# Optimization experiments

Measured on AMD Instinct MI355X. Metric: run time of the kernel, lower is better.

Reference implementation:

```python
import jax, jax.numpy as jnp
import numpy as np

N = 100000      # nodes
E = 1600000     # edges
IN_DIM = 500
HID = 64
OUT = 40
BN_EPS = 1e-5


def setup_inputs() -> dict:
    key = jax.random.key(0)
    ks = jax.random.split(key, 20)
    x = jax.random.normal(ks[0], (N, IN_DIM), dtype=jnp.float32)
    edge_index = jax.random.randint(ks[1], (2, E), 0, N, dtype=jnp.int64)

    def lin(k, fin, fout):
        return jax.random.normal(k, (fin, fout), dtype=jnp.float32) / np.sqrt(fin).astype(np.float32)

    inp = {
        "x": x,
        "edge_index": edge_index,
        "W1": lin(ks[2], IN_DIM, HID),
        "b1": jnp.zeros((HID,), jnp.float32),
        "g1": jnp.ones((HID,), jnp.float32),
        "be1": jnp.zeros((HID,), jnp.float32),
        "m1": 0.1 * jax.random.normal(ks[3], (HID,), jnp.float32),
        "v1": jax.random.uniform(ks[4], (HID,), jnp.float32, 0.5, 1.5),
        "W2": lin(ks[5], HID, HID),
        "b2": jnp.zeros((HID,), jnp.float32),
        "g2": jnp.ones((HID,), jnp.float32),
        "be2": jnp.zeros((HID,), jnp.float32),
        "m2": 0.1 * jax.random.normal(ks[6], (HID,), jnp.float32),
        "v2": jax.random.uniform(ks[7], (HID,), jnp.float32, 0.5, 1.5),
        "W3": lin(ks[8], HID, OUT),
        "b3": jnp.zeros((OUT,), jnp.float32),
    }
    return inp


def _gcn_conv(h, src, dst, deg_inv_sqrt, W, b):
    # PyG GCNConv (add_self_loops=True, normalize=True, eval math):
    # out = D^-1/2 (A + I) D^-1/2 (h @ W) + b
    h = h @ W                                    # [N, F]
    norm = deg_inv_sqrt[src] * deg_inv_sqrt[dst]  # [E]
    msg = h[src] * norm[:, None]                  # [E, F] gather
    agg = jax.ops.segment_sum(msg, dst, num_segments=N)  # scatter-add
    agg = agg + h * (deg_inv_sqrt * deg_inv_sqrt)[:, None]  # self-loop term
    return agg + b


def reference(x, edge_index, W1, b1, g1, be1, m1, v1,
              W2, b2, g2, be2, m2, v2, W3, b3):
    src, dst = edge_index[0], edge_index[1]
    # degree including self-loop
    deg = jax.ops.segment_sum(jnp.ones((E,), x.dtype), dst, num_segments=N) + 1.0
    deg_inv_sqrt = jax.lax.rsqrt(deg)

    def bn(h, g, be, m, v):
        return (h - m) * jax.lax.rsqrt(v + BN_EPS) * g + be

    h = _gcn_conv(x, src, dst, deg_inv_sqrt, W1, b1)
    h = jax.nn.relu(bn(h, g1, be1, m1, v1))
    # dropout: identity in eval mode
    h = _gcn_conv(h, src, dst, deg_inv_sqrt, W2, b2)
    h = jax.nn.relu(bn(h, g2, be2, m2, v2))
    out = _gcn_conv(h, src, dst, deg_inv_sqrt, W3, b3)
    return jax.nn.log_softmax(out, axis=1)
```

## Files before the change

kernel.cpp:

```cpp
#include <hip/hip_runtime.h>
#include <math.h>

#define N_NODES 100000
#define N_EDGES 1600000
#define IN_DIM  500
#define HID     64
#define OUT_DIM 40
#define BN_EPS  1e-5f
#define SCAN_NB 98
#define NTILE   6250

typedef _Float16 f16;
typedef __attribute__((ext_vector_type(2))) _Float16 f16x2;
typedef __attribute__((ext_vector_type(8))) _Float16 f16x8;
typedef __attribute__((ext_vector_type(4))) float f32x4;

static inline int cdiv(long a, int b) { return (int)((a + b - 1) / b); }

__device__ inline unsigned short f2h_bits(float f) {
    f16 h = (f16)f;
    return __builtin_bit_cast(unsigned short, h);
}
__device__ inline f16x2 bits2h2(unsigned int u) {
    return __builtin_bit_cast(f16x2, u);
}

__global__ void k_count_deg(const int* __restrict__ ei, int* degi) {
    int e = blockIdx.x * 256 + threadIdx.x;
    if (e < N_EDGES) atomicAdd(&degi[ei[N_EDGES + e]], 1);
}

__global__ void k_scan1(const int* __restrict__ degi, int* __restrict__ rowptr,
                        int* __restrict__ blocksum, float* __restrict__ dis) {
    __shared__ int sd[256];
    int tid = threadIdx.x;
    int base = blockIdx.x * 1024 + tid * 4;
    int v0 = (base + 0 < N_NODES) ? degi[base + 0] : -1;
    int v1 = (base + 1 < N_NODES) ? degi[base + 1] : -1;
    int v2 = (base + 2 < N_NODES) ? degi[base + 2] : -1;
    int v3 = (base + 3 < N_NODES) ? degi[base + 3] : -1;
    if (base + 0 < N_NODES) dis[base + 0] = rsqrtf((float)v0 + 1.0f);
    if (base + 1 < N_NODES) dis[base + 1] = rsqrtf((float)v1 + 1.0f);
    if (base + 2 < N_NODES) dis[base + 2] = rsqrtf((float)v2 + 1.0f);
    if (base + 3 < N_NODES) dis[base + 3] = rsqrtf((float)v3 + 1.0f);
    int w0 = v0 + 1, w1 = v1 + 1, w2 = v2 + 1, w3 = v3 + 1;
    int s = w0 + w1 + w2 + w3;
    sd[tid] = s;
    __syncthreads();
    for (int off = 1; off < 256; off <<= 1) {
        int t = (tid >= off) ? sd[tid - off] : 0;
        __syncthreads();
        sd[tid] += t;
        __syncthreads();
    }
    int excl = sd[tid] - s;
    if (base + 0 < N_NODES) rowptr[base + 0] = excl;
    if (base + 1 < N_NODES) rowptr[base + 1] = excl + w0;
    if (base + 2 < N_NODES) rowptr[base + 2] = excl + w0 + w1;
    if (base + 3 < N_NODES) rowptr[base + 3] = excl + w0 + w1 + w2;
    if (tid == 255) blocksum[blockIdx.x] = sd[255];
}

__global__ void k_scan2(int* __restrict__ blocksum, int* __restrict__ blockbase) {
    __shared__ int sd[128];
    int tid = threadIdx.x;
    int v = (tid < SCAN_NB) ? blocksum[tid] : 0;
    sd[tid] = v;
    __syncthreads();
    for (int off = 1; off < 128; off <<= 1) {
        int t = (tid >= off) ? sd[tid - off] : 0;
        __syncthreads();
        sd[tid] += t;
        __syncthreads();
    }
    if (tid < SCAN_NB) blockbase[tid] = sd[tid] - v;
}

__global__ void k_scan3(int* __restrict__ rowptr, const int* __restrict__ blockbase,
                        const int* __restrict__ degi, int* __restrict__ cursor,
                        uint2* __restrict__ epack) {
    int add = blockbase[blockIdx.x];
    int base = blockIdx.x * 1024 + threadIdx.x * 4;
#pragma unroll
    for (int i = 0; i < 4; ++i) {
        int node = base + i;
        if (node < N_NODES) {
            int rp = rowptr[node] + add;
            rowptr[node] = rp;
            float d2 = 1.0f / (float)(degi[node] + 1);
            unsigned int hb = f2h_bits(d2);
            epack[rp] = make_uint2((unsigned int)(node * 128), (hb << 16) | hb);
            cursor[node] = 1;
        }
    }
    if (blockIdx.x == 0 && threadIdx.x == 0)
        rowptr[N_NODES] = N_EDGES + N_NODES;
}

__global__ void k_permute(const int* __restrict__ ei, const int* __restrict__ rowptr,
                          int* __restrict__ cursor, const float* __restrict__ dis,
                          uint2* __restrict__ epack) {
    int e = blockIdx.x * 256 + threadIdx.x;
    if (e >= N_EDGES) return;
    int s = ei[e];
    int d = ei[N_EDGES + e];
    int pos = rowptr[d] + atomicAdd(&cursor[d], 1);
    unsigned int hb = f2h_bits(dis[s] * dis[d]);
    epack[pos] = make_uint2((unsigned int)(s * 128), (hb << 16) | hb);
}

__device__ inline void convW_one(const float* W, unsigned short* wb,
                                 int idx, int K, int F) {
    int j    = idx & 7;
    int lane = (idx >> 3) & 63;
    int q    = idx >> 9;
    int t    = q >> 2, nt = q & 3;
    int n = nt * 16 + (lane & 15);
    int k = t * 32 + ((lane >> 4) << 3) + j;
    float v = (k < K && n < F) ? W[(long)k * F + n] : 0.f;
    wb[idx] = f2h_bits(v);
}

__global__ void k_convall(const float* __restrict__ W1, const float* __restrict__ W2,
                          const float* __restrict__ W3,
                          unsigned short* __restrict__ wb1,
                          unsigned short* __restrict__ wb2,
                          unsigned short* __restrict__ wb3) {
    int idx = blockIdx.x * 256 + threadIdx.x;
    if (idx < 32768) {
        convW_one(W1, wb1, idx, IN_DIM, HID);
    } else if (idx < 36864) {
        convW_one(W2, wb2, idx - 32768, HID, HID);
    } else {
        convW_one(W3, wb3, idx - 36864, HID, OUT_DIM);
    }
}

__global__ void k_bnfold(const float* __restrict__ b1, const float* __restrict__ g1,
                         const float* __restrict__ be1, const float* __restrict__ m1,
                         const float* __restrict__ v1,
                         const float* __restrict__ b2, const float* __restrict__ g2,
                         const float* __restrict__ be2, const float* __restrict__ m2,
                         const float* __restrict__ v2,
                         unsigned short* __restrict__ sc1,
                         unsigned short* __restrict__ sc2) {
    int t = threadIdx.x;
    int c = t & 63;
    const float *b, *g, *be, *m, *v;
    unsigned short* sc;
    if (t < 64) { b = b1; g = g1; be = be1; m = m1; v = v1; sc = sc1; }
    else        { b = b2; g = g2; be = be2; m = m2; v = v2; sc = sc2; }
    float S = g[c] * rsqrtf(v[c] + BN_EPS);
    float C = (b[c] - m[c]) * S + be[c];
    sc[c]      = f2h_bits(S);
    sc[64 + c] = f2h_bits(C);
}

__global__ __launch_bounds__(256) void k_l1fused(
        const float* __restrict__ x,
        const unsigned short* __restrict__ wb,
        unsigned short* __restrict__ h) {
    __shared__ unsigned short l[16 * 520];
    const int rt = blockIdx.x;
    const int tid = threadIdx.x;

#pragma unroll
    for (int it = 0; it < 8; ++it) {
        int slot = it * 256 + tid;
        int row = slot >> 7, kq = slot & 127;
        float4 v = make_float4(0.f, 0.f, 0.f, 0.f);
        if (kq < 125)
            v = *reinterpret_cast<const float4*>(x + ((long)rt * 16 + row) * IN_DIM + kq * 4);
        unsigned int u0 = (unsigned int)f2h_bits(v.x) | ((unsigned int)f2h_bits(v.y) << 16);
        unsigned int u1 = (unsigned int)f2h_bits(v.z) | ((unsigned int)f2h_bits(v.w) << 16);
        *reinterpret_cast<uint2*>(&l[row * 520 + kq * 4]) = make_uint2(u0, u1);
    }
    __syncthreads();

    const int wid  = tid >> 6;
    const int lane = tid & 63;
    const int l15  = lane & 15;
    const int lhi  = lane >> 4;

    const f16x8* bp = reinterpret_cast<const f16x8*>(wb) + wid * 64 + lane;
    const unsigned short* arow = &l[l15 * 520 + lhi * 8];

    f32x4 acc = (f32x4){0.f, 0.f, 0.f, 0.f};
    f16x8 ca = *reinterpret_cast<const f16x8*>(arow);
    f16x8 cb = bp[0];

#pragma unroll
    for (int t = 0; t < 16; ++t) {
        f16x8 na, nb;
        if (t < 15) {
            na = *reinterpret_cast<const f16x8*>(arow + (t + 1) * 32);
            nb = bp[(t + 1) * 256];
        }
        acc = __builtin_amdgcn_mfma_f32_16x16x32_f16(ca, cb, acc, 0, 0, 0);
        if (t < 15) { ca = na; cb = nb; }
    }

#pragma unroll
    for (int rr = 0; rr < 4; ++rr) {
        long grow = (long)rt * 16 + lhi * 4 + rr;
        h[grow * 64 + wid * 16 + l15] = f2h_bits(acc[rr]);
    }
}

__global__ __launch_bounds__(256) void k_agg_gemm(
        const unsigned short* __restrict__ h_in, const int* __restrict__ rowptr,
        const uint2* __restrict__ epack, const unsigned short* __restrict__ sc,
        const unsigned short* __restrict__ wb, unsigned short* __restrict__ h_out) {
    __shared__ unsigned short st[16 * 80];
    const int base = blockIdx.x * 16;
    const int tid  = threadIdx.x;
    const int wid  = tid >> 6;
    const int lane = tid & 63;
    const int e8 = lane >> 3, c8 = lane & 7;
    const int node0 = base + wid * 4;

    int start[4], cnt[4];
    {
        int r0 = rowptr[node0 + 0], r1 = rowptr[node0 + 1], r2 = rowptr[node0 + 2];
        int r3 = rowptr[node0 + 3], r4 = rowptr[node0 + 4];
        start[0] = r0; cnt[0] = r1 - r0;
        start[1] = r1; cnt[1] = r2 - r1;
        start[2] = r2; cnt[2] = r3 - r2;
        start[3] = r3; cnt[3] = r4 - r3;
    }
    const char* hb = (const char*)h_in + c8 * 16;

    f16x2 a[4][4];
#pragma unroll
    for (int s = 0; s < 4; ++s)
#pragma unroll
        for (int i = 0; i < 4; ++i) a[s][i] = (f16x2)0;

    int maxc = max(max(cnt[0], cnt[1]), max(cnt[2], cnt[3]));

    for (int j = 0; j < maxc; j += 8) {
        int jj = j + e8;
#pragma unroll
        for (int s = 0; s < 4; ++s) {
            bool valid = jj < cnt[s];
            uint2 mv = epack[start[s] + (valid ? jj : 0)];
            f16x2 w2 = bits2h2(valid ? mv.y : 0u);
            uint4 hv = *(const uint4*)(hb + mv.x);
            a[s][0] += bits2h2(hv.x) * w2;
            a[s][1] += bits2h2(hv.y) * w2;
            a[s][2] += bits2h2(hv.z) * w2;
            a[s][3] += bits2h2(hv.w) * w2;
        }
    }

#pragma unroll
    for (int off = 8; off < 64; off <<= 1) {
#pragma unroll
        for (int s = 0; s < 4; ++s)
#pragma unroll
            for (int i = 0; i < 4; ++i) {
                unsigned int u = __builtin_bit_cast(unsigned int, a[s][i]);
                a[s][i] += bits2h2((unsigned int)__shfl_xor((int)u, off));
            }
    }

    if (e8 == 0) {
        uint4 Su = *(const uint4*)(sc + c8 * 8);
        uint4 Cu = *(const uint4*)(sc + 64 + c8 * 8);
        unsigned int sw[4] = {Su.x, Su.y, Su.z, Su.w};
        unsigned int cw[4] = {Cu.x, Cu.y, Cu.z, Cu.w};
#pragma unroll
        for (int s = 0; s < 4; ++s) {
            unsigned int u[4];
#pragma unroll
            for (int p = 0; p < 4; ++p) {
                f16x2 r = a[s][p] * bits2h2(sw[p]) + bits2h2(cw[p]);
                r[0] = r[0] > (f16)0 ? r[0] : (f16)0;
                r[1] = r[1] > (f16)0 ? r[1] : (f16)0;
                u[p] = __builtin_bit_cast(unsigned int, r);
            }
            int row = wid * 4 + s;
            *reinterpret_cast<uint4*>(&st[row * 80 + c8 * 8]) =
                make_uint4(u[0], u[1], u[2], u[3]);
        }
    }
    __syncthreads();

    const int l15 = lane & 15, lhi = lane >> 4;
    const unsigned short* arow = &st[l15 * 80 + lhi * 8];
    const f16x8* bp = reinterpret_cast<const f16x8*>(wb) + wid * 64 + lane;

    f32x4 acc = (f32x4){0.f, 0.f, 0.f, 0.f};
    f16x8 a0 = *reinterpret_cast<const f16x8*>(arow);
    f16x8 a1 = *reinterpret_cast<const f16x8*>(arow + 32);
    f16x8 b0 = bp[0];
    f16x8 b1 = bp[256];
    acc = __builtin_amdgcn_mfma_f32_16x16x32_f16(a0, b0, acc, 0, 0, 0);
    acc = __builtin_amdgcn_mfma_f32_16x16x32_f16(a1, b1, acc, 0, 0, 0);

#pragma unroll
    for (int rr = 0; rr < 4; ++rr) {
        long grow = (long)base + lhi * 4 + rr;
        h_out[grow * 64 + wid * 16 + l15] = f2h_bits(acc[rr]);
    }
}

__global__ __launch_bounds__(256) void k_agg_lsm(
        const unsigned short* __restrict__ h, const int* __restrict__ rowptr,
        const uint2* __restrict__ epack,
        const float* __restrict__ bias, float* __restrict__ out) {
    int node = blockIdx.x * 4 + (threadIdx.x >> 6);
    if (node >= N_NODES) return;
    const int lane = threadIdx.x & 63;
    const int e8 = lane >> 3, c8 = lane & 7;
    const bool okc = c8 < 5;

    const int start = rowptr[node];
    const int cnt   = rowptr[node + 1] - start;
    const uint2* ep = epack + start;
    const char*  hb = (const char*)h + c8 * 16;

    f16x2 a[4] = {(f16x2)0, (f16x2)0, (f16x2)0, (f16x2)0};

    auto batch = [&](int j) {
        int jj = j + e8;
        bool valid = jj < cnt;
        uint2 mv = ep[valid ? jj : 0];
        f16x2 w2 = bits2h2((valid && okc) ? mv.y : 0u);
        uint4 hv = *(const uint4*)(hb + (okc ? mv.x : 0u));
        a[0] += bits2h2(hv.x) * w2;
        a[1] += bits2h2(hv.y) * w2;
        a[2] += bits2h2(hv.z) * w2;
        a[3] += bits2h2(hv.w) * w2;
    };

    batch(0);
    if (cnt > 8)  batch(8);
    if (cnt > 16) batch(16);
    if (cnt > 24) batch(24);
    for (int j = 32; j < cnt; j += 8) batch(j);

#pragma unroll
    for (int off = 8; off < 64; off <<= 1) {
#pragma unroll
        for (int i = 0; i < 4; ++i) {
            unsigned int u = __builtin_bit_cast(unsigned int, a[i]);
            a[i] += bits2h2((unsigned int)__shfl_xor((int)u, off));
        }
    }

    float av[8] = {(float)a[0][0], (float)a[0][1], (float)a[1][0], (float)a[1][1],
                   (float)a[2][0], (float)a[2][1], (float)a[3][0], (float)a[3][1]};
    float vals[8];
    float mx = -INFINITY;
    if (okc) {
        float4 bb0 = *(const float4*)(bias + c8 * 8), bb1 = *(const float4*)(bias + c8 * 8 + 4);
        float bbv[8] = {bb0.x, bb0.y, bb0.z, bb0.w, bb1.x, bb1.y, bb1.z, bb1.w};
#pragma unroll
        for (int i = 0; i < 8; ++i) {
            vals[i] = av[i] + bbv[i];
            mx = fmaxf(mx, vals[i]);
        }
    }
#pragma unroll
    for (int o = 1; o < 8; o <<= 1) mx = fmaxf(mx, __shfl_xor(mx, o));
    float es = 0.f;
    if (okc) {
#pragma unroll
        for (int i = 0; i < 8; ++i) es += expf(vals[i] - mx);
    }
#pragma unroll
    for (int o = 1; o < 8; o <<= 1) es += __shfl_xor(es, o);
    float ls = logf(es);

    if (e8 == 0 && okc) {
        float* op = out + (long)node * 40 + c8 * 8;
        *(float4*)op = make_float4(vals[0] - mx - ls, vals[1] - mx - ls,
                                   vals[2] - mx - ls, vals[3] - mx - ls);
        *(float4*)(op + 4) = make_float4(vals[4] - mx - ls, vals[5] - mx - ls,
                                         vals[6] - mx - ls, vals[7] - mx - ls);
    }
}

extern "C" void kernel_launch(void* const* d_in, const int* in_sizes, int n_in,
                              void* d_out, int out_size, void* d_ws, size_t ws_size,
                              hipStream_t stream) {
    const float* x   = (const float*)d_in[0];
    const int*   ei  = (const int*)d_in[1];
    const float* W1  = (const float*)d_in[2];
    const float* b1  = (const float*)d_in[3];
    const float* g1  = (const float*)d_in[4];
    const float* be1 = (const float*)d_in[5];
    const float* m1  = (const float*)d_in[6];
    const float* v1  = (const float*)d_in[7];
    const float* W2  = (const float*)d_in[8];
    const float* b2  = (const float*)d_in[9];
    const float* g2  = (const float*)d_in[10];
    const float* be2 = (const float*)d_in[11];
    const float* m2  = (const float*)d_in[12];
    const float* v2  = (const float*)d_in[13];
    const float* W3  = (const float*)d_in[14];
    const float* b3  = (const float*)d_in[15];
    float* out = (float*)d_out;

    float* ws        = (float*)d_ws;
    float* dis       = ws;
    int*   degi      = (int*)(ws + 100096);
    int*   cursor    = (int*)(ws + 200192);
    int*   rowptr    = (int*)(ws + 300288);
    int*   blocksum  = (int*)(ws + 400384);
    int*   blockbase = (int*)(ws + 400512);
    uint2* epack     = (uint2*)(ws + 400640);
    unsigned short* h1 = (unsigned short*)(ws + 3800640);
    unsigned short* h2 = (unsigned short*)(ws + 7000640);
    unsigned short* h3 = (unsigned short*)(ws + 10200640);
    unsigned short* wb1 = (unsigned short*)(ws + 13400640);
    unsigned short* wb2 = (unsigned short*)(ws + 13417024);
    unsigned short* wb3 = (unsigned short*)(ws + 13419072);
    unsigned short* sc1 = (unsigned short*)(ws + 13421120);
    unsigned short* sc2 = sc1 + 128;

    hipMemsetAsync(degi, 0, 100096 * sizeof(int), stream);
    k_count_deg<<<cdiv(N_EDGES, 256), 256, 0, stream>>>(ei, degi);
    k_scan1<<<SCAN_NB, 256, 0, stream>>>(degi, rowptr, blocksum, dis);
    k_scan2<<<1, 128, 0, stream>>>(blocksum, blockbase);
    k_scan3<<<SCAN_NB, 256, 0, stream>>>(rowptr, blockbase, degi, cursor, epack);
    k_permute<<<cdiv(N_EDGES, 256), 256, 0, stream>>>(ei, rowptr, cursor, dis, epack);

    k_convall<<<160, 256, 0, stream>>>(W1, W2, W3, wb1, wb2, wb3);
    k_bnfold<<<1, 128, 0, stream>>>(b1, g1, be1, m1, v1, b2, g2, be2, m2, v2, sc1, sc2);

    const int agg_grid = cdiv(N_NODES, 4);

    k_l1fused<<<NTILE, 256, 0, stream>>>(x, wb1, h1);

    k_agg_gemm<<<NTILE, 256, 0, stream>>>(h1, rowptr, epack, sc1, wb2, h2);

    k_agg_gemm<<<NTILE, 256, 0, stream>>>(h2, rowptr, epack, sc2, wb3, h3);

    k_agg_lsm<<<agg_grid, 256, 0, stream>>>(h3, rowptr, epack, b3, out);
}
```

Before: 335.4 us.

## Overlap layer-1 GEMM with CSR build phases and restructure aggregation loop

Splits the layer-1 dense projection into three chunks and co-schedules each chunk in the same launch as a graph preprocessing phase: degree counting, the scan finalize, and the edge permutation. The latency-bound atomic phases can then overlap with the bandwidth-heavy x read. Weight conversion and BN folding are merged into one launch, cutting launch count. The aggregation loop now walks each node's edges separately instead of iterating all four nodes up to the max degree, which avoids padded gathers but loses interleaved memory-level parallelism across nodes.

```diff
diff --git a/kernel.cpp b/kernel.cpp
--- a/kernel.cpp
+++ b/kernel.cpp
@@ -9,6 +9,10 @@
 #define BN_EPS  1e-5f
 #define SCAN_NB 98
 #define NTILE   6250
+#define EBLK    6250
+#define L1A     2500
+#define L1B     1250
+#define L1C     2500
 
 typedef _Float16 f16;
 typedef __attribute__((ext_vector_type(2))) _Float16 f16x2;
@@ -23,11 +27,6 @@
 }
 __device__ inline f16x2 bits2h2(unsigned int u) {
     return __builtin_bit_cast(f16x2, u);
-}
-
-__global__ void k_count_deg(const int* __restrict__ ei, int* degi) {
-    int e = blockIdx.x * 256 + threadIdx.x;
-    if (e < N_EDGES) atomicAdd(&degi[ei[N_EDGES + e]], 1);
 }
 
 __global__ void k_scan1(const int* __restrict__ degi, int* __restrict__ rowptr,
@@ -76,11 +75,12 @@
     if (tid < SCAN_NB) blockbase[tid] = sd[tid] - v;
 }
 
-__global__ void k_scan3(int* __restrict__ rowptr, const int* __restrict__ blockbase,
-                        const int* __restrict__ degi, int* __restrict__ cursor,
-                        uint2* __restrict__ epack) {
-    int add = blockbase[blockIdx.x];
-    int base = blockIdx.x * 1024 + threadIdx.x * 4;
+__device__ inline void dev_scan3(int bid, int tid, int* __restrict__ rowptr,
+                                 const int* __restrict__ blockbase,
+                                 const int* __restrict__ degi, int* __restrict__ cursor,
+                                 uint2* __restrict__ epack) {
+    int add = blockbase[bid];
+    int base = bid * 1024 + tid * 4;
 #pragma unroll
     for (int i = 0; i < 4; ++i) {
         int node = base + i;
@@ -93,20 +93,107 @@
             cursor[node] = 1;
         }
     }
-    if (blockIdx.x == 0 && threadIdx.x == 0)
+    if (bid == 0 && tid == 0)
         rowptr[N_NODES] = N_EDGES + N_NODES;
 }
 
-__global__ void k_permute(const int* __restrict__ ei, const int* __restrict__ rowptr,
-                          int* __restrict__ cursor, const float* __restrict__ dis,
-                          uint2* __restrict__ epack) {
-    int e = blockIdx.x * 256 + threadIdx.x;
-    if (e >= N_EDGES) return;
-    int s = ei[e];
-    int d = ei[N_EDGES + e];
-    int pos = rowptr[d] + atomicAdd(&cursor[d], 1);
-    unsigned int hb = f2h_bits(dis[s] * dis[d]);
-    epack[pos] = make_uint2((unsigned int)(s * 128), (hb << 16) | hb);
+__device__ inline void dev_l1fused(int rt, int tid,
+                                   const float* __restrict__ x,
+                                   const unsigned short* __restrict__ wb,
+                                   unsigned short* __restrict__ h,
+                                   unsigned short* l ) {
+#pragma unroll
+    for (int it = 0; it < 8; ++it) {
+        int slot = it * 256 + tid;
+        int row = slot >> 7, kq = slot & 127;
+        float4 v = make_float4(0.f, 0.f, 0.f, 0.f);
+        if (kq < 125)
+            v = *reinterpret_cast<const float4*>(x + ((long)rt * 16 + row) * IN_DIM + kq * 4);
+        unsigned int u0 = (unsigned int)f2h_bits(v.x) | ((unsigned int)f2h_bits(v.y) << 16);
+        unsigned int u1 = (unsigned int)f2h_bits(v.z) | ((unsigned int)f2h_bits(v.w) << 16);
+        *reinterpret_cast<uint2*>(&l[row * 520 + kq * 4]) = make_uint2(u0, u1);
+    }
+    __syncthreads();
+
+    const int wid  = tid >> 6;
+    const int lane = tid & 63;
+    const int l15  = lane & 15;
+    const int lhi  = lane >> 4;
+
+    const f16x8* bp = reinterpret_cast<const f16x8*>(wb) + wid * 64 + lane;
+    const unsigned short* arow = &l[l15 * 520 + lhi * 8];
+
+    f32x4 acc = (f32x4){0.f, 0.f, 0.f, 0.f};
+    f16x8 ca = *reinterpret_cast<const f16x8*>(arow);
+    f16x8 cb = bp[0];
+
+#pragma unroll
+    for (int t = 0; t < 16; ++t) {
+        f16x8 na, nb;
+        if (t < 15) {
+            na = *reinterpret_cast<const f16x8*>(arow + (t + 1) * 32);
+            nb = bp[(t + 1) * 256];
+        }
+        acc = __builtin_amdgcn_mfma_f32_16x16x32_f16(ca, cb, acc, 0, 0, 0);
+        if (t < 15) { ca = na; cb = nb; }
+    }
+
+#pragma unroll
+    for (int rr = 0; rr < 4; ++rr) {
+        long grow = (long)rt * 16 + lhi * 4 + rr;
+        h[grow * 64 + wid * 16 + l15] = f2h_bits(acc[rr]);
+    }
+}
+
+__global__ __launch_bounds__(256) void k_front1(
+        const float* __restrict__ x, const unsigned short* __restrict__ wb1,
+        unsigned short* __restrict__ h1,
+        const int* __restrict__ ei, int* __restrict__ degi) {
+    __shared__ unsigned short l[16 * 520];
+    int b = blockIdx.x;
+    if (b < L1A) {
+        dev_l1fused(b, threadIdx.x, x, wb1, h1, l);
+    } else {
+        int e = (b - L1A) * 256 + threadIdx.x;
+        if (e < N_EDGES) atomicAdd(&degi[ei[N_EDGES + e]], 1);
+    }
+}
+
+__global__ __launch_bounds__(256) void k_front2(
+        const float* __restrict__ x, const unsigned short* __restrict__ wb1,
+        unsigned short* __restrict__ h1,
+        int* __restrict__ rowptr, const int* __restrict__ blockbase,
+        const int* __restrict__ degi, int* __restrict__ cursor,
+        uint2* __restrict__ epack) {
+    __shared__ unsigned short l[16 * 520];
+    int b = blockIdx.x;
+    if (b < L1B) {
+        dev_l1fused(L1A + b, threadIdx.x, x, wb1, h1, l);
+    } else {
+        dev_scan3(b - L1B, threadIdx.x, rowptr, blockbase, degi, cursor, epack);
+    }
+}
+
+__global__ __launch_bounds__(256) void k_front3(
+        const float* __restrict__ x, const unsigned short* __restrict__ wb1,
+        unsigned short* __restrict__ h1,
+        const int* __restrict__ ei, const int* __restrict__ rowptr,
+        int* __restrict__ cursor, const float* __restrict__ dis,
+        uint2* __restrict__ epack) {
+    __shared__ unsigned short l[16 * 520];
+    int b = blockIdx.x;
+    if (b < L1C) {
+        dev_l1fused(L1A + L1B + b, threadIdx.x, x, wb1, h1, l);
+    } else {
+        int e = (b - L1C) * 256 + threadIdx.x;
+        if (e < N_EDGES) {
+            int s = ei[e];
+            int d = ei[N_EDGES + e];
+            int pos = rowptr[d] + atomicAdd(&cursor[d], 1);
+            unsigned int hb = f2h_bits(dis[s] * dis[d]);
+            epack[pos] = make_uint2((unsigned int)(s * 128), (hb << 16) | hb);
+        }
+    }
 }
 
 __device__ inline void convW_one(const float* W, unsigned short* wb,
@@ -121,11 +208,34 @@
     wb[idx] = f2h_bits(v);
 }
 
-__global__ void k_convall(const float* __restrict__ W1, const float* __restrict__ W2,
-                          const float* __restrict__ W3,
-                          unsigned short* __restrict__ wb1,
-                          unsigned short* __restrict__ wb2,
-                          unsigned short* __restrict__ wb3) {
+__global__ void k_conv(const float* __restrict__ W1, const float* __restrict__ W2,
+                       const float* __restrict__ W3,
+                       unsigned short* __restrict__ wb1,
+                       unsigned short* __restrict__ wb2,
+                       unsigned short* __restrict__ wb3,
+                       const float* __restrict__ b1, const float* __restrict__ g1,
+                       const float* __restrict__ be1, const float* __restrict__ m1,
+                       const float* __restrict__ v1,
+                       const float* __restrict__ b2, const float* __restrict__ g2,
+                       const float* __restrict__ be2, const float* __restrict__ m2,
+                       const float* __restrict__ v2,
+                       unsigned short* __restrict__ sc1,
+                       unsigned short* __restrict__ sc2) {
+    if (blockIdx.x == 160) {
+        int t = threadIdx.x;
+        if (t < 128) {
+            int c = t & 63;
+            const float *b, *g, *be, *m, *v;
+            unsigned short* sc;
+            if (t < 64) { b = b1; g = g1; be = be1; m = m1; v = v1; sc = sc1; }
+            else        { b = b2; g = g2; be = be2; m = m2; v = v2; sc = sc2; }
+            float S = g[c] * rsqrtf(v[c] + BN_EPS);
+            float C = (b[c] - m[c]) * S + be[c];
+            sc[c]      = f2h_bits(S);
+            sc[64 + c] = f2h_bits(C);
+        }
+        return;
+    }
     int idx = blockIdx.x * 256 + threadIdx.x;
     if (idx < 32768) {
         convW_one(W1, wb1, idx, IN_DIM, HID);
@@ -133,77 +243,6 @@
         convW_one(W2, wb2, idx - 32768, HID, HID);
     } else {
         convW_one(W3, wb3, idx - 36864, HID, OUT_DIM);
-    }
-}
-
-__global__ void k_bnfold(const float* __restrict__ b1, const float* __restrict__ g1,
-                         const float* __restrict__ be1, const float* __restrict__ m1,
-                         const float* __restrict__ v1,
-                         const float* __restrict__ b2, const float* __restrict__ g2,
-                         const float* __restrict__ be2, const float* __restrict__ m2,
-                         const float* __restrict__ v2,
-                         unsigned short* __restrict__ sc1,
-                         unsigned short* __restrict__ sc2) {
-    int t = threadIdx.x;
-    int c = t & 63;
-    const float *b, *g, *be, *m, *v;
-    unsigned short* sc;
-    if (t < 64) { b = b1; g = g1; be = be1; m = m1; v = v1; sc = sc1; }
-    else        { b = b2; g = g2; be = be2; m = m2; v = v2; sc = sc2; }
-    float S = g[c] * rsqrtf(v[c] + BN_EPS);
-    float C = (b[c] - m[c]) * S + be[c];
-    sc[c]      = f2h_bits(S);
-    sc[64 + c] = f2h_bits(C);
-}
-
-__global__ __launch_bounds__(256) void k_l1fused(
-        const float* __restrict__ x,
-        const unsigned short* __restrict__ wb,
-        unsigned short* __restrict__ h) {
-    __shared__ unsigned short l[16 * 520];
-    const int rt = blockIdx.x;
-    const int tid = threadIdx.x;
-
-#pragma unroll
-    for (int it = 0; it < 8; ++it) {
-        int slot = it * 256 + tid;
-        int row = slot >> 7, kq = slot & 127;
-        float4 v = make_float4(0.f, 0.f, 0.f, 0.f);
-        if (kq < 125)
-            v = *reinterpret_cast<const float4*>(x + ((long)rt * 16 + row) * IN_DIM + kq * 4);
-        unsigned int u0 = (unsigned int)f2h_bits(v.x) | ((unsigned int)f2h_bits(v.y) << 16);
-        unsigned int u1 = (unsigned int)f2h_bits(v.z) | ((unsigned int)f2h_bits(v.w) << 16);
-        *reinterpret_cast<uint2*>(&l[row * 520 + kq * 4]) = make_uint2(u0, u1);
-    }
-    __syncthreads();
-
-    const int wid  = tid >> 6;
-    const int lane = tid & 63;
-    const int l15  = lane & 15;
-    const int lhi  = lane >> 4;
-
-    const f16x8* bp = reinterpret_cast<const f16x8*>(wb) + wid * 64 + lane;
-    const unsigned short* arow = &l[l15 * 520 + lhi * 8];
-
-    f32x4 acc = (f32x4){0.f, 0.f, 0.f, 0.f};
-    f16x8 ca = *reinterpret_cast<const f16x8*>(arow);
-    f16x8 cb = bp[0];
-
-#pragma unroll
-    for (int t = 0; t < 16; ++t) {
-        f16x8 na, nb;
-        if (t < 15) {
-            na = *reinterpret_cast<const f16x8*>(arow + (t + 1) * 32);
-            nb = bp[(t + 1) * 256];
-        }
-        acc = __builtin_amdgcn_mfma_f32_16x16x32_f16(ca, cb, acc, 0, 0, 0);
-        if (t < 15) { ca = na; cb = nb; }
-    }
-
-#pragma unroll
-    for (int rr = 0; rr < 4; ++rr) {
-        long grow = (long)rt * 16 + lhi * 4 + rr;
-        h[grow * 64 + wid * 16 + l15] = f2h_bits(acc[rr]);
     }
 }
 
@@ -236,21 +275,25 @@
 #pragma unroll
         for (int i = 0; i < 4; ++i) a[s][i] = (f16x2)0;
 
-    int maxc = max(max(cnt[0], cnt[1]), max(cnt[2], cnt[3]));
-
-    for (int j = 0; j < maxc; j += 8) {
+    auto gath = [&](int s, int j) {
         int jj = j + e8;
-#pragma unroll
-        for (int s = 0; s < 4; ++s) {
-            bool valid = jj < cnt[s];
-            uint2 mv = epack[start[s] + (valid ? jj : 0)];
-            f16x2 w2 = bits2h2(valid ? mv.y : 0u);
-            uint4 hv = *(const uint4*)(hb + mv.x);
-            a[s][0] += bits2h2(hv.x) * w2;
-            a[s][1] += bits2h2(hv.y) * w2;
-            a[s][2] += bits2h2(hv.z) * w2;
-            a[s][3] += bits2h2(hv.w) * w2;
-        }
+        bool valid = jj < cnt[s];
+        uint2 mv = epack[start[s] + (valid ? jj : 0)];
+        f16x2 w2 = bits2h2(valid ? mv.y : 0u);
+        uint4 hv = *(const uint4*)(hb + mv.x);
+        a[s][0] += bits2h2(hv.x) * w2;
+        a[s][1] += bits2h2(hv.y) * w2;
+        a[s][2] += bits2h2(hv.z) * w2;
+        a[s][3] += bits2h2(hv.w) * w2;
+    };
+
+#pragma unroll
+    for (int s = 0; s < 4; ++s) {
+        gath(s, 0);
+        if (cnt[s] > 8)  gath(s, 8);
+        if (cnt[s] > 16) gath(s, 16);
+        if (cnt[s] > 24) gath(s, 24);
+        for (int j = 32; j < cnt[s]; j += 8) gath(s, j);
     }
 
 #pragma unroll
@@ -421,22 +464,24 @@
     unsigned short* sc2 = sc1 + 128;
 
     hipMemsetAsync(degi, 0, 100096 * sizeof(int), stream);
-    k_count_deg<<<cdiv(N_EDGES, 256), 256, 0, stream>>>(ei, degi);
+
+    k_conv<<<161, 256, 0, stream>>>(W1, W2, W3, wb1, wb2, wb3,
+                                    b1, g1, be1, m1, v1, b2, g2, be2, m2, v2,
+                                    sc1, sc2);
+
+    k_front1<<<L1A + EBLK, 256, 0, stream>>>(x, wb1, h1, ei, degi);
+
     k_scan1<<<SCAN_NB, 256, 0, stream>>>(degi, rowptr, blocksum, dis);
     k_scan2<<<1, 128, 0, stream>>>(blocksum, blockbase);
-    k_scan3<<<SCAN_NB, 256, 0, stream>>>(rowptr, blockbase, degi, cursor, epack);
-    k_permute<<<cdiv(N_EDGES, 256), 256, 0, stream>>>(ei, rowptr, cursor, dis, epack);
-
-    k_convall<<<160, 256, 0, stream>>>(W1, W2, W3, wb1, wb2, wb3);
-    k_bnfold<<<1, 128, 0, stream>>>(b1, g1, be1, m1, v1, b2, g2, be2, m2, v2, sc1, sc2);
-
-    const int agg_grid = cdiv(N_NODES, 4);
-
-    k_l1fused<<<NTILE, 256, 0, stream>>>(x, wb1, h1);
+
+    k_front2<<<L1B + SCAN_NB, 256, 0, stream>>>(x, wb1, h1, rowptr, blockbase,
+                                                degi, cursor, epack);
+
+    k_front3<<<L1C + EBLK, 256, 0, stream>>>(x, wb1, h1, ei, rowptr, cursor,
+                                             dis, epack);
 
     k_agg_gemm<<<NTILE, 256, 0, stream>>>(h1, rowptr, epack, sc1, wb2, h2);
-
     k_agg_gemm<<<NTILE, 256, 0, stream>>>(h2, rowptr, epack, sc2, wb3, h3);
 
-    k_agg_lsm<<<agg_grid, 256, 0, stream>>>(h3, rowptr, epack, b3, out);
-}
+    k_agg_lsm<<<cdiv(N_NODES, 4), 256, 0, stream>>>(h3, rowptr, epack, b3, out);
+}
```

Measured after the change: 347.9 us. 3.7% more time.
